# Optimization experiments

Hardware: AMD Instinct MI355X
Metric: run time of the kernel (lower is better)

Reference implementation:

```python
import jax, jax.numpy as jnp
import numpy as np

B, C, H, W = 2, 128, 64, 64
HEADS, DHEAD = 4, 32
K = 7           # kernel_size (dilation = 1)
GROUPS = 32
EPS = 1e-5
DA = HEADS * DHEAD


def setup_inputs() -> dict:
    key = jax.random.key(0)
    ks = jax.random.split(key, 8)
    s = lambda k, sh: jax.random.normal(k, sh, jnp.float32) * 0.02
    return {
        "x": jax.random.normal(ks[0], (B, C, H, W), jnp.float32),
        "gn_weight": jnp.ones((C,), jnp.float32),
        "gn_bias": jnp.zeros((C,), jnp.float32),
        "wq": s(ks[1], (DA, C)), "bq": jnp.zeros((DA,), jnp.float32),
        "wk": s(ks[2], (DA, C)), "bk": jnp.zeros((DA,), jnp.float32),
        "wv": s(ks[3], (DA, C)), "bv": jnp.zeros((DA,), jnp.float32),
        "wo": s(ks[4], (C, DA)), "bo": jnp.zeros((C,), jnp.float32),
        "rpb": s(ks[5], (HEADS, 2 * K - 1, 2 * K - 1)),
    }


def _win_starts(L):
    # NATTEN window start: clamp so the k-window stays in-bounds
    return jnp.clip(jnp.arange(L) - K // 2, 0, L - K)


def _pb_starts(L):
    # NATTEN relative-position-bias start index along one axis
    idx = jnp.arange(L)
    ns = K // 2
    return ns + jnp.maximum(ns - idx, 0) + jnp.minimum(L - idx - 1 - ns, 0)


def reference(x, gn_weight, gn_bias, wq, bq, wk, bk, wv, bv, wo, bo, rpb):
    Bn, Cn, Hn, Wn = x.shape
    # GroupNorm (biased variance, like torch)
    xg = x.reshape(Bn, GROUPS, -1)
    mu = xg.mean(-1, keepdims=True)
    var = xg.var(-1, keepdims=True)
    xg = (xg - mu) * jax.lax.rsqrt(var + EPS)
    xn = xg.reshape(Bn, Cn, Hn, Wn) * gn_weight[:, None, None] + gn_bias[:, None, None]

    def proj(w, b):
        # 1x1 conv == channel matmul; -> (B, heads, H, W, d)
        y = jnp.einsum('bchw,oc->bohw', xn, w) + b[:, None, None]
        return y.reshape(Bn, HEADS, DHEAD, Hn, Wn).transpose(0, 1, 3, 4, 2)

    q = proj(wq, bq) * (DHEAD ** -0.5)
    k = proj(wk, bk)
    v = proj(wv, bv)

    off = jnp.arange(K)
    ih = _win_starts(Hn)[:, None] + off        # (H, K) neighbor rows
    iw = _win_starts(Wn)[:, None] + off        # (W, K) neighbor cols
    # gathered windows: (B, heads, H, W, K, K, d)
    kw = k[:, :, ih[:, None, :, None], iw[None, :, None, :], :]
    vw = v[:, :, ih[:, None, :, None], iw[None, :, None, :], :]

    bh = _pb_starts(Hn)[:, None] + off         # (H, K)
    bw = _pb_starts(Wn)[:, None] + off         # (W, K)
    bias = rpb[:, bh[:, None, :, None], bw[None, :, None, :]]  # (heads, H, W, K, K)

    attn = jnp.einsum('nhpqd,nhpqijd->nhpqij', q, kw) + bias[None]
    attn = jax.nn.softmax(attn.reshape(Bn, HEADS, Hn, Wn, K * K), axis=-1)
    attn = attn.reshape(Bn, HEADS, Hn, Wn, K, K)
    out = jnp.einsum('nhpqij,nhpqijd->nhpqd', attn, vw)  # (B, heads, H, W, d)
    # faithful to the torch code: raw reshape (B,heads,H,W,d)->(B,H,W,heads*d)
    xo = out.reshape(Bn, Hn, Wn, HEADS * DHEAD).transpose(0, 3, 1, 2)
    return jnp.einsum('bchw,oc->bohw', xo, wo) + bo[:, None, None]
```

## Files before the change

### kernel.cpp

```cpp
#include <hip/hip_runtime.h>

#define EPS 1e-5f

typedef short s8v __attribute__((ext_vector_type(8)));
typedef float f4v __attribute__((ext_vector_type(4)));

static __device__ inline short f2bf(float f) {
  return __builtin_bit_cast(short, (__bf16)f);
}

#define OFF_S     0
#define OFF_T     256
#define OFF_WCB   512
#define OFF_BC    (OFF_WCB + 24576)
#define OFF_QB    (OFF_BC + 384)
#define OFF_KB    (OFF_QB + 524288)
#define OFF_VTB   (OFF_KB + 524288)
#define OFF_WOB   (OFF_VTB + 524288)

__global__ __launch_bounds__(256) void kP(
    const float* __restrict__ wq, const float* __restrict__ bq,
    const float* __restrict__ wk, const float* __restrict__ bk,
    const float* __restrict__ wv, const float* __restrict__ bv,
    const float* __restrict__ wo, const float* __restrict__ gw,
    const float* __restrict__ gb, const float* __restrict__ x,
    short* __restrict__ Wcb, float* __restrict__ bc,
    short* __restrict__ WoB, float* __restrict__ sArr, float* __restrict__ tArr) {
  int blk = blockIdx.x;
  if (blk < 64) {
    int t = blk * 256 + threadIdx.x;
    const float qs = 0.17677669529663687f;
    Wcb[t]         = f2bf(wq[t] * qs);
    Wcb[16384 + t] = f2bf(wk[t]);
    Wcb[32768 + t] = f2bf(wv[t]);
    WoB[t]         = f2bf(wo[t]);
    if (t < 128) {
      bc[t]       = bq[t] * qs;
      bc[128 + t] = bk[t];
      bc[256 + t] = bv[t];
    }
  } else {
    int g = blk - 64;
    const float4* xp = (const float4*)(x + (size_t)g * 16384);
    float s = 0.f, s2 = 0.f;
    for (int i = threadIdx.x; i < 4096; i += 256) {
      float4 v = xp[i];
      s  += v.x + v.y + v.z + v.w;
      s2 += v.x*v.x + v.y*v.y + v.z*v.z + v.w*v.w;
    }
    #pragma unroll
    for (int o = 32; o; o >>= 1) {
      s  += __shfl_down(s, o, 64);
      s2 += __shfl_down(s2, o, 64);
    }
    __shared__ float ls[4], ls2[4];
    int wid = threadIdx.x >> 6, lane = threadIdx.x & 63;
    if (!lane) { ls[wid] = s; ls2[wid] = s2; }
    __syncthreads();
    if (threadIdx.x == 0) {
      float S = 0.f, S2 = 0.f;
      #pragma unroll
      for (int i = 0; i < 4; i++) { S += ls[i]; S2 += ls2[i]; }
      float mean = S * (1.f / 16384.f);
      float var  = S2 * (1.f / 16384.f) - mean * mean;
      float rsv  = rsqrtf(var + EPS);
      int b = g >> 5, grp = g & 31;
      #pragma unroll
      for (int j = 0; j < 4; j++) {
        int c = grp * 4 + j;
        float sv = rsv * gw[c];
        sArr[b * 128 + c] = sv;
        tArr[b * 128 + c] = gb[c] - mean * sv;
      }
    }
  }
}

__global__ __launch_bounds__(256) void k2_qkv(
    const float* __restrict__ x, const float* __restrict__ sArr, const float* __restrict__ tArr,
    const short* __restrict__ Wcb, const float* __restrict__ bc,
    short* __restrict__ qb, short* __restrict__ kb, short* __restrict__ vtb) {
  __shared__ short xn[64][136];
  __shared__ short WL[192][136];
  __shared__ float bcs[192];
  int bid    = blockIdx.x;
  int ptile  = bid >> 1, nslice = bid & 1;
  int b      = ptile >> 6;
  int pbase  = (ptile & 63) * 64;
  int nbase  = nslice * 192;
  int tid    = threadIdx.x;
  int w      = __builtin_amdgcn_readfirstlane(tid >> 6);
  int lane   = tid & 63;

  #pragma unroll
  for (int i = 0; i < 16; i++) {
    int c0 = (w + i * 4) * 2;
    float s0 = sArr[b * 128 + c0],     t0 = tArr[b * 128 + c0];
    float s1 = sArr[b * 128 + c0 + 1], t1 = tArr[b * 128 + c0 + 1];
    float v0 = x[((size_t)(b * 128 + c0))     * 4096 + pbase + lane];
    float v1 = x[((size_t)(b * 128 + c0 + 1)) * 4096 + pbase + lane];
    ushort e0 = (ushort)f2bf(fmaf(v0, s0, t0));
    ushort e1 = (ushort)f2bf(fmaf(v1, s1, t1));
    *(uint*)&xn[lane][c0] = ((uint)e1 << 16) | e0;
  }
  #pragma unroll
  for (int i = 0; i < 12; i++) {
    int cc = tid + i * 256;
    int row = cc >> 4, c8 = (cc & 15) * 8;
    *(s8v*)&WL[row][c8] = *(const s8v*)&Wcb[(nbase + row) * 128 + c8];
  }
  if (tid < 192) bcs[tid] = bc[nbase + tid];
  __syncthreads();

  int l15 = lane & 15, kh = lane >> 4;
  f4v acc[12];
  #pragma unroll
  for (int nt = 0; nt < 12; nt++) acc[nt] = (f4v){0.f, 0.f, 0.f, 0.f};
  #pragma unroll
  for (int ks = 0; ks < 4; ks++) {
    s8v a = *(s8v*)&xn[w * 16 + l15][ks * 32 + kh * 8];
    #pragma unroll
    for (int nt = 0; nt < 12; nt++) {
      s8v wf = *(s8v*)&WL[nt * 16 + l15][ks * 32 + kh * 8];
      if (nbase + nt * 16 < 256)
        acc[nt] = __builtin_amdgcn_mfma_f32_16x16x32_bf16(wf, a, acc[nt], 0, 0, 0);
      else
        acc[nt] = __builtin_amdgcn_mfma_f32_16x16x32_bf16(a, wf, acc[nt], 0, 0, 0);
    }
  }
  #pragma unroll
  for (int nt = 0; nt < 12; nt++) {
    if (nbase + nt * 16 < 256) {
      int ob  = nt * 16 + kh * 4;
      int o0i = nbase + ob;
      int hd  = (o0i & 127) >> 5, d0 = o0i & 31;
      int bh2 = b * 4 + hd;
      int px  = pbase + w * 16 + l15;
      short* dst = (o0i >> 7) ? kb : qb;
      ushort e0 = (ushort)f2bf(acc[nt][0] + bcs[ob + 0]);
      ushort e1 = (ushort)f2bf(acc[nt][1] + bcs[ob + 1]);
      ushort e2 = (ushort)f2bf(acc[nt][2] + bcs[ob + 2]);
      ushort e3 = (ushort)f2bf(acc[nt][3] + bcs[ob + 3]);
      uint2 pk = make_uint2(((uint)e1 << 16) | e0, ((uint)e3 << 16) | e2);
      *(uint2*)&dst[((size_t)bh2 * 4096 + px) * 32 + d0] = pk;
    } else {
      int o   = nbase + nt * 16 + l15;
      int hd  = (o & 127) >> 5, d = o & 31;
      int bh2 = b * 4 + hd;
      int px0 = pbase + w * 16 + kh * 4;
      float bias = bcs[nt * 16 + l15];
      ushort s0 = (ushort)f2bf(acc[nt][0] + bias);
      ushort s1 = (ushort)f2bf(acc[nt][1] + bias);
      ushort s2 = (ushort)f2bf(acc[nt][2] + bias);
      ushort s3 = (ushort)f2bf(acc[nt][3] + bias);
      uint2 pk2 = make_uint2(((uint)s1 << 16) | s0, ((uint)s3 << 16) | s2);
      *(uint2*)&vtb[((size_t)bh2 * 32 + d) * 4096 + px0] = pk2;
    }
  }
}

__global__ __launch_bounds__(512) void k3_attn_proj(
    const short* __restrict__ qb, const short* __restrict__ kb, const short* __restrict__ vtb,
    const float* __restrict__ rpb, const short* __restrict__ WoB,
    const float* __restrict__ bo, float* __restrict__ out) {
  struct PhA { ushort K[8][64][32]; ushort VT[8][32][68]; ushort P[8][16][40]; float rpb[176]; };
  struct PhB { ushort tile[2][16][136]; ushort Wo[128][136]; };
  __shared__ union { PhA a; PhB bb; } sm;

  int lb    = blockIdx.x;
  int bh    = lb & 7;
  int chunk = lb >> 3;
  int y0    = chunk * 2;
  int head  = bh & 3, b = bh >> 2;
  int tid   = threadIdx.x;
  int w     = __builtin_amdgcn_readfirstlane(tid >> 6);
  int lane  = tid & 63, l15 = lane & 15, kh = lane >> 4;
  int wsub  = w & 3, rsel = w >> 2;
  int y     = y0 + rsel;
  int ys0   = min(max(y0 - 3, 0), 57);
  int ysoff = min(max(y - 3, 0), 57) - ys0;

  {
    const size_t kbase = (size_t)bh * 4096 * 32;
    #pragma unroll
    for (int i = 0; i < 4; i++) {
      int cc = tid + i * 512;
      int row = cc >> 8, rem = cc & 255;
      int col = rem >> 2, ch8 = (rem & 3) * 8;
      int yr = min(ys0 + row, 63);
      *(s8v*)&sm.a.K[row][col][ch8] = *(const s8v*)&kb[kbase + (size_t)(yr * 64 + col) * 32 + ch8];
    }
  }
  {
    const size_t vbase = (size_t)bh * 32 * 4096;
    #pragma unroll
    for (int i = 0; i < 4; i++) {
      int cc = tid + i * 512;
      int row = cc >> 8, rem = cc & 255;
      int d = rem >> 3, c8 = (rem & 7) * 8;
      int yr = min(ys0 + row, 63);
      *(s8v*)&sm.a.VT[row][d][c8] = *(const s8v*)&vtb[vbase + (size_t)d * 4096 + yr * 64 + c8];
    }
  }
  if (tid < 169) sm.a.rpb[tid] = rpb[head * 169 + tid];
  __syncthreads();

  int c0  = wsub * 8 + (wsub >> 1) * 8;
  int xq  = wsub * 16 + l15;
  int xs  = min(max(xq - 3, 0), 57);
  int pbw = 3 + max(3 - xq, 0) + min(60 - xq, 0);
  int pbh = 3 + max(3 - y, 0) + min(60 - y, 0);

  s8v qf = *(const s8v*)&qb[((size_t)bh * 4096 + y * 64 + xq) * 32 + kh * 8];

  int   bidx[8];
  float badd[8];
  #pragma unroll
  for (int j = 0; j < 8; ++j) {
    int cc = (j >> 2) * 16 + kh * 4 + (j & 3);
    int dx = c0 + cc - xs;
    bool valid = (dx >= 0) && (dx < 7);
    bidx[j] = pbw + min(max(dx, 0), 6);
    badd[j] = valid ? 0.f : -1e30f;
  }

  const f4v zero = {0.f, 0.f, 0.f, 0.f};
  f4v o0 = zero, o1 = zero;
  float ssum = 0.f;

  #pragma unroll
  for (int row = 0; row < 7; ++row) {
    int kr = ysoff + row;
    s8v ka0 = *(s8v*)&sm.a.K[kr][c0 + l15][kh * 8];
    s8v ka1 = *(s8v*)&sm.a.K[kr][c0 + 16 + l15][kh * 8];
    f4v lg0 = __builtin_amdgcn_mfma_f32_16x16x32_bf16(ka0, qf, zero, 0, 0, 0);
    f4v lg1 = __builtin_amdgcn_mfma_f32_16x16x32_bf16(ka1, qf, zero, 0, 0, 0);
    int rbase = (pbh + row) * 13;
    float p[8];
    #pragma unroll
    for (int j = 0; j < 4; ++j) {
      p[j]     = __expf(lg0[j] + sm.a.rpb[rbase + bidx[j]]     + badd[j]);
      p[j + 4] = __expf(lg1[j] + sm.a.rpb[rbase + bidx[j + 4]] + badd[j + 4]);
      ssum += p[j] + p[j + 4];
    }
    uint u0 = ((uint)(ushort)f2bf(p[1]) << 16) | (ushort)f2bf(p[0]);
    uint u1 = ((uint)(ushort)f2bf(p[3]) << 16) | (ushort)f2bf(p[2]);
    uint u2 = ((uint)(ushort)f2bf(p[5]) << 16) | (ushort)f2bf(p[4]);
    uint u3 = ((uint)(ushort)f2bf(p[7]) << 16) | (ushort)f2bf(p[6]);
    *(uint2*)&sm.a.P[w][l15][kh * 4]      = make_uint2(u0, u1);
    *(uint2*)&sm.a.P[w][l15][16 + kh * 4] = make_uint2(u2, u3);
    s8v pa  = *(s8v*)&sm.a.P[w][l15][kh * 8];
    s8v vt0 = *(s8v*)&sm.a.VT[kr][l15][c0 + kh * 8];
    s8v vt1 = *(s8v*)&sm.a.VT[kr][16 + l15][c0 + kh * 8];
    o0 = __builtin_amdgcn_mfma_f32_16x16x32_bf16(pa, vt0, o0, 0, 0, 0);
    o1 = __builtin_amdgcn_mfma_f32_16x16x32_bf16(pa, vt1, o1, 0, 0, 0);
  }

  ssum += __shfl_xor(ssum, 16, 64);
  ssum += __shfl_xor(ssum, 32, 64);

  __syncthreads();

  #pragma unroll
  for (int i = 0; i < 4; i++) {
    int cc = tid + i * 512;
    int row = cc >> 4, c8 = (cc & 15) * 8;
    *(s8v*)&sm.bb.Wo[row][c8] = *(const s8v*)&WoB[row * 128 + c8];
  }
  {
    int col = wsub * 4 + kh;
    #pragma unroll
    for (int r = 0; r < 4; ++r) {
      float sq = __builtin_bit_cast(float,
          __builtin_amdgcn_ds_bpermute((kh * 4 + r) << 2, __builtin_bit_cast(int, ssum)));
      float inv = 1.f / sq;
      sm.bb.tile[rsel][col][r * 32 + l15]      = (ushort)f2bf(o0[r] * inv);
      sm.bb.tile[rsel][col][r * 32 + 16 + l15] = (ushort)f2bf(o1[r] * inv);
    }
  }
  __syncthreads();

  f4v acc2[2];
  acc2[0] = zero; acc2[1] = zero;
  #pragma unroll
  for (int ks = 0; ks < 4; ks++) {
    s8v a = *(s8v*)&sm.bb.tile[rsel][l15][ks * 32 + kh * 8];
    #pragma unroll
    for (int nt = 0; nt < 2; nt++) {
      s8v bf = *(s8v*)&sm.bb.Wo[wsub * 32 + nt * 16 + l15][ks * 32 + kh * 8];
      acc2[nt] = __builtin_amdgcn_mfma_f32_16x16x32_bf16(a, bf, acc2[nt], 0, 0, 0);
    }
  }
  int pxg = (head * 16 + (y >> 2)) * 64 + ((y & 3) << 4);
  #pragma unroll
  for (int nt = 0; nt < 2; nt++) {
    int o = wsub * 32 + nt * 16 + l15;
    float bias = bo[o];
    float4 val = make_float4(acc2[nt][0] + bias, acc2[nt][1] + bias,
                             acc2[nt][2] + bias, acc2[nt][3] + bias);
    *(float4*)&out[((size_t)b * 128 + o) * 4096 + pxg + kh * 4] = val;
  }
}

extern "C" void kernel_launch(void* const* d_in, const int* in_sizes, int n_in,
                              void* d_out, int out_size, void* d_ws, size_t ws_size,
                              hipStream_t stream) {
  (void)in_sizes; (void)n_in; (void)out_size; (void)ws_size;
  const float* x   = (const float*)d_in[0];
  const float* gw  = (const float*)d_in[1];
  const float* gb  = (const float*)d_in[2];
  const float* wq  = (const float*)d_in[3];
  const float* bq  = (const float*)d_in[4];
  const float* wk  = (const float*)d_in[5];
  const float* bk  = (const float*)d_in[6];
  const float* wv  = (const float*)d_in[7];
  const float* bv  = (const float*)d_in[8];
  const float* wo  = (const float*)d_in[9];
  const float* bo  = (const float*)d_in[10];
  const float* rpb = (const float*)d_in[11];
  float* ws    = (float*)d_ws;
  float* sArr  = ws + OFF_S;
  float* tArr  = ws + OFF_T;
  short* Wcb   = (short*)(ws + OFF_WCB);
  float* bc    = ws + OFF_BC;
  short* qb    = (short*)(ws + OFF_QB);
  short* kb    = (short*)(ws + OFF_KB);
  short* vtb   = (short*)(ws + OFF_VTB);
  short* WoB   = (short*)(ws + OFF_WOB);
  float* out   = (float*)d_out;

  hipLaunchKernelGGL(kP, dim3(128), dim3(256), 0, stream,
                     wq, bq, wk, bk, wv, bv, wo, gw, gb, x, Wcb, bc, WoB, sArr, tArr);
  hipLaunchKernelGGL(k2_qkv, dim3(256), dim3(256), 0, stream,
                     x, sArr, tArr, Wcb, bc, qb, kb, vtb);
  hipLaunchKernelGGL(k3_attn_proj, dim3(256), dim3(512), 0, stream,
                     qb, kb, vtb, rpb, WoB, bo, out);
}
```

Baseline: 32.36 us.

## Split GroupNorm stats into partial sums, finalize in QKV kernel, preload Wo

```diff
diff --git a/kernel.cpp b/kernel.cpp
--- a/kernel.cpp
+++ b/kernel.cpp
@@ -9,8 +9,8 @@
   return __builtin_bit_cast(short, (__bf16)f);
 }
 
-#define OFF_S     0
-#define OFF_T     256
+#define OFF_SP    0
+#define OFF_S2P   256
 #define OFF_WCB   512
 #define OFF_BC    (OFF_WCB + 24576)
 #define OFF_QB    (OFF_BC + 384)
@@ -22,13 +22,13 @@
     const float* __restrict__ wq, const float* __restrict__ bq,
     const float* __restrict__ wk, const float* __restrict__ bk,
     const float* __restrict__ wv, const float* __restrict__ bv,
-    const float* __restrict__ wo, const float* __restrict__ gw,
-    const float* __restrict__ gb, const float* __restrict__ x,
+    const float* __restrict__ wo, const float* __restrict__ x,
     short* __restrict__ Wcb, float* __restrict__ bc,
-    short* __restrict__ WoB, float* __restrict__ sArr, float* __restrict__ tArr) {
+    short* __restrict__ WoB, float* __restrict__ Spart, float* __restrict__ S2part) {
   int blk = blockIdx.x;
+  int tid = threadIdx.x;
   if (blk < 64) {
-    int t = blk * 256 + threadIdx.x;
+    int t = blk * 256 + tid;
     const float qs = 0.17677669529663687f;
     Wcb[t]         = f2bf(wq[t] * qs);
     Wcb[16384 + t] = f2bf(wk[t]);
@@ -40,11 +40,13 @@
       bc[256 + t] = bv[t];
     }
   } else {
-    int g = blk - 64;
-    const float4* xp = (const float4*)(x + (size_t)g * 16384);
+    int idx = blk - 64;
+    int g = idx >> 2, part = idx & 3;
+    const float4* xp = (const float4*)(x + (size_t)g * 16384 + part * 4096);
     float s = 0.f, s2 = 0.f;
-    for (int i = threadIdx.x; i < 4096; i += 256) {
-      float4 v = xp[i];
+    #pragma unroll
+    for (int i = 0; i < 4; i++) {
+      float4 v = xp[tid + i * 256];
       s  += v.x + v.y + v.z + v.w;
       s2 += v.x*v.x + v.y*v.y + v.z*v.z + v.w*v.w;
     }
@@ -54,35 +56,29 @@
       s2 += __shfl_down(s2, o, 64);
     }
     __shared__ float ls[4], ls2[4];
-    int wid = threadIdx.x >> 6, lane = threadIdx.x & 63;
+    int wid = tid >> 6, lane = tid & 63;
     if (!lane) { ls[wid] = s; ls2[wid] = s2; }
     __syncthreads();
-    if (threadIdx.x == 0) {
+    if (tid == 0) {
       float S = 0.f, S2 = 0.f;
       #pragma unroll
       for (int i = 0; i < 4; i++) { S += ls[i]; S2 += ls2[i]; }
-      float mean = S * (1.f / 16384.f);
-      float var  = S2 * (1.f / 16384.f) - mean * mean;
-      float rsv  = rsqrtf(var + EPS);
-      int b = g >> 5, grp = g & 31;
-      #pragma unroll
-      for (int j = 0; j < 4; j++) {
-        int c = grp * 4 + j;
-        float sv = rsv * gw[c];
-        sArr[b * 128 + c] = sv;
-        tArr[b * 128 + c] = gb[c] - mean * sv;
-      }
+      Spart[idx]  = S;
+      S2part[idx] = S2;
     }
   }
 }
 
 __global__ __launch_bounds__(256) void k2_qkv(
-    const float* __restrict__ x, const float* __restrict__ sArr, const float* __restrict__ tArr,
+    const float* __restrict__ x,
+    const float* __restrict__ Spart, const float* __restrict__ S2part,
+    const float* __restrict__ gw, const float* __restrict__ gb,
     const short* __restrict__ Wcb, const float* __restrict__ bc,
     short* __restrict__ qb, short* __restrict__ kb, short* __restrict__ vtb) {
   __shared__ short xn[64][136];
   __shared__ short WL[192][136];
   __shared__ float bcs[192];
+  __shared__ float sm_s[128], sm_t[128];
   int bid    = blockIdx.x;
   int ptile  = bid >> 1, nslice = bid & 1;
   int b      = ptile >> 6;
@@ -92,16 +88,22 @@
   int w      = __builtin_amdgcn_readfirstlane(tid >> 6);
   int lane   = tid & 63;
 
+  float va[16], vb[16];
   #pragma unroll
   for (int i = 0; i < 16; i++) {
     int c0 = (w + i * 4) * 2;
-    float s0 = sArr[b * 128 + c0],     t0 = tArr[b * 128 + c0];
-    float s1 = sArr[b * 128 + c0 + 1], t1 = tArr[b * 128 + c0 + 1];
-    float v0 = x[((size_t)(b * 128 + c0))     * 4096 + pbase + lane];
-    float v1 = x[((size_t)(b * 128 + c0 + 1)) * 4096 + pbase + lane];
-    ushort e0 = (ushort)f2bf(fmaf(v0, s0, t0));
-    ushort e1 = (ushort)f2bf(fmaf(v1, s1, t1));
-    *(uint*)&xn[lane][c0] = ((uint)e1 << 16) | e0;
+    va[i] = x[((size_t)(b * 128 + c0))     * 4096 + pbase + lane];
+    vb[i] = x[((size_t)(b * 128 + c0 + 1)) * 4096 + pbase + lane];
+  }
+  if (tid < 128) {
+    int c = tid, gi = (b * 32 + (c >> 2)) * 4;
+    float S  = Spart[gi]  + Spart[gi + 1]  + Spart[gi + 2]  + Spart[gi + 3];
+    float S2 = S2part[gi] + S2part[gi + 1] + S2part[gi + 2] + S2part[gi + 3];
+    float mean = S * (1.f / 16384.f);
+    float var  = S2 * (1.f / 16384.f) - mean * mean;
+    float sv   = rsqrtf(var + EPS) * gw[c];
+    sm_s[c] = sv;
+    sm_t[c] = gb[c] - mean * sv;
   }
   #pragma unroll
   for (int i = 0; i < 12; i++) {
@@ -110,6 +112,15 @@
     *(s8v*)&WL[row][c8] = *(const s8v*)&Wcb[(nbase + row) * 128 + c8];
   }
   if (tid < 192) bcs[tid] = bc[nbase + tid];
+  __syncthreads();
+
+  #pragma unroll
+  for (int i = 0; i < 16; i++) {
+    int c0 = (w + i * 4) * 2;
+    ushort e0 = (ushort)f2bf(fmaf(va[i], sm_s[c0],     sm_t[c0]));
+    ushort e1 = (ushort)f2bf(fmaf(vb[i], sm_s[c0 + 1], sm_t[c0 + 1]));
+    *(uint*)&xn[lane][c0] = ((uint)e1 << 16) | e0;
+  }
   __syncthreads();
 
   int l15 = lane & 15, kh = lane >> 4;
@@ -163,9 +174,12 @@
     const short* __restrict__ qb, const short* __restrict__ kb, const short* __restrict__ vtb,
     const float* __restrict__ rpb, const short* __restrict__ WoB,
     const float* __restrict__ bo, float* __restrict__ out) {
-  struct PhA { ushort K[8][64][32]; ushort VT[8][32][68]; ushort P[8][16][40]; float rpb[176]; };
-  struct PhB { ushort tile[2][16][136]; ushort Wo[128][136]; };
-  __shared__ union { PhA a; PhB bb; } sm;
+  __shared__ ushort K_s[8][64][32];
+  __shared__ ushort VT_s[8][32][68];
+  __shared__ ushort P_s[8][16][40];
+  __shared__ ushort Wo_s[128][136];
+  __shared__ ushort tile_s[2][16][136];
+  __shared__ float  rpb_s[176];
 
   int lb    = blockIdx.x;
   int bh    = lb & 7;
@@ -188,7 +202,7 @@
       int row = cc >> 8, rem = cc & 255;
       int col = rem >> 2, ch8 = (rem & 3) * 8;
       int yr = min(ys0 + row, 63);
-      *(s8v*)&sm.a.K[row][col][ch8] = *(const s8v*)&kb[kbase + (size_t)(yr * 64 + col) * 32 + ch8];
+      *(s8v*)&K_s[row][col][ch8] = *(const s8v*)&kb[kbase + (size_t)(yr * 64 + col) * 32 + ch8];
     }
   }
   {
@@ -199,10 +213,16 @@
       int row = cc >> 8, rem = cc & 255;
       int d = rem >> 3, c8 = (rem & 7) * 8;
       int yr = min(ys0 + row, 63);
-      *(s8v*)&sm.a.VT[row][d][c8] = *(const s8v*)&vtb[vbase + (size_t)d * 4096 + yr * 64 + c8];
-    }
-  }
-  if (tid < 169) sm.a.rpb[tid] = rpb[head * 169 + tid];
+      *(s8v*)&VT_s[row][d][c8] = *(const s8v*)&vtb[vbase + (size_t)d * 4096 + yr * 64 + c8];
+    }
+  }
+  #pragma unroll
+  for (int i = 0; i < 4; i++) {
+    int cc = tid + i * 512;
+    int row = cc >> 4, c8 = (cc & 15) * 8;
+    *(s8v*)&Wo_s[row][c8] = *(const s8v*)&WoB[row * 128 + c8];
+  }
+  if (tid < 169) rpb_s[tid] = rpb[head * 169 + tid];
   __syncthreads();
 
   int c0  = wsub * 8 + (wsub >> 1) * 8;
@@ -231,27 +251,27 @@
   #pragma unroll
   for (int row = 0; row < 7; ++row) {
     int kr = ysoff + row;
-    s8v ka0 = *(s8v*)&sm.a.K[kr][c0 + l15][kh * 8];
-    s8v ka1 = *(s8v*)&sm.a.K[kr][c0 + 16 + l15][kh * 8];
+    s8v ka0 = *(s8v*)&K_s[kr][c0 + l15][kh * 8];
+    s8v ka1 = *(s8v*)&K_s[kr][c0 + 16 + l15][kh * 8];
     f4v lg0 = __builtin_amdgcn_mfma_f32_16x16x32_bf16(ka0, qf, zero, 0, 0, 0);
     f4v lg1 = __builtin_amdgcn_mfma_f32_16x16x32_bf16(ka1, qf, zero, 0, 0, 0);
     int rbase = (pbh + row) * 13;
     float p[8];
     #pragma unroll
     for (int j = 0; j < 4; ++j) {
-      p[j]     = __expf(lg0[j] + sm.a.rpb[rbase + bidx[j]]     + badd[j]);
-      p[j + 4] = __expf(lg1[j] + sm.a.rpb[rbase + bidx[j + 4]] + badd[j + 4]);
+      p[j]     = __expf(lg0[j] + rpb_s[rbase + bidx[j]]     + badd[j]);
+      p[j + 4] = __expf(lg1[j] + rpb_s[rbase + bidx[j + 4]] + badd[j + 4]);
       ssum += p[j] + p[j + 4];
     }
     uint u0 = ((uint)(ushort)f2bf(p[1]) << 16) | (ushort)f2bf(p[0]);
     uint u1 = ((uint)(ushort)f2bf(p[3]) << 16) | (ushort)f2bf(p[2]);
     uint u2 = ((uint)(ushort)f2bf(p[5]) << 16) | (ushort)f2bf(p[4]);
     uint u3 = ((uint)(ushort)f2bf(p[7]) << 16) | (ushort)f2bf(p[6]);
-    *(uint2*)&sm.a.P[w][l15][kh * 4]      = make_uint2(u0, u1);
-    *(uint2*)&sm.a.P[w][l15][16 + kh * 4] = make_uint2(u2, u3);
-    s8v pa  = *(s8v*)&sm.a.P[w][l15][kh * 8];
-    s8v vt0 = *(s8v*)&sm.a.VT[kr][l15][c0 + kh * 8];
-    s8v vt1 = *(s8v*)&sm.a.VT[kr][16 + l15][c0 + kh * 8];
+    *(uint2*)&P_s[w][l15][kh * 4]      = make_uint2(u0, u1);
+    *(uint2*)&P_s[w][l15][16 + kh * 4] = make_uint2(u2, u3);
+    s8v pa  = *(s8v*)&P_s[w][l15][kh * 8];
+    s8v vt0 = *(s8v*)&VT_s[kr][l15][c0 + kh * 8];
+    s8v vt1 = *(s8v*)&VT_s[kr][16 + l15][c0 + kh * 8];
     o0 = __builtin_amdgcn_mfma_f32_16x16x32_bf16(pa, vt0, o0, 0, 0, 0);
     o1 = __builtin_amdgcn_mfma_f32_16x16x32_bf16(pa, vt1, o1, 0, 0, 0);
   }
@@ -259,14 +279,6 @@
   ssum += __shfl_xor(ssum, 16, 64);
   ssum += __shfl_xor(ssum, 32, 64);
 
-  __syncthreads();
-
-  #pragma unroll
-  for (int i = 0; i < 4; i++) {
-    int cc = tid + i * 512;
-    int row = cc >> 4, c8 = (cc & 15) * 8;
-    *(s8v*)&sm.bb.Wo[row][c8] = *(const s8v*)&WoB[row * 128 + c8];
-  }
   {
     int col = wsub * 4 + kh;
     #pragma unroll
@@ -274,8 +286,8 @@
       float sq = __builtin_bit_cast(float,
           __builtin_amdgcn_ds_bpermute((kh * 4 + r) << 2, __builtin_bit_cast(int, ssum)));
       float inv = 1.f / sq;
-      sm.bb.tile[rsel][col][r * 32 + l15]      = (ushort)f2bf(o0[r] * inv);
-      sm.bb.tile[rsel][col][r * 32 + 16 + l15] = (ushort)f2bf(o1[r] * inv);
+      tile_s[rsel][col][r * 32 + l15]      = (ushort)f2bf(o0[r] * inv);
+      tile_s[rsel][col][r * 32 + 16 + l15] = (ushort)f2bf(o1[r] * inv);
     }
   }
   __syncthreads();
@@ -284,10 +296,10 @@
   acc2[0] = zero; acc2[1] = zero;
   #pragma unroll
   for (int ks = 0; ks < 4; ks++) {
-    s8v a = *(s8v*)&sm.bb.tile[rsel][l15][ks * 32 + kh * 8];
+    s8v a = *(s8v*)&tile_s[rsel][l15][ks * 32 + kh * 8];
     #pragma unroll
     for (int nt = 0; nt < 2; nt++) {
-      s8v bf = *(s8v*)&sm.bb.Wo[wsub * 32 + nt * 16 + l15][ks * 32 + kh * 8];
+      s8v bf = *(s8v*)&Wo_s[wsub * 32 + nt * 16 + l15][ks * 32 + kh * 8];
       acc2[nt] = __builtin_amdgcn_mfma_f32_16x16x32_bf16(a, bf, acc2[nt], 0, 0, 0);
     }
   }
@@ -318,21 +330,21 @@
   const float* wo  = (const float*)d_in[9];
   const float* bo  = (const float*)d_in[10];
   const float* rpb = (const float*)d_in[11];
-  float* ws    = (float*)d_ws;
-  float* sArr  = ws + OFF_S;
-  float* tArr  = ws + OFF_T;
-  short* Wcb   = (short*)(ws + OFF_WCB);
-  float* bc    = ws + OFF_BC;
-  short* qb    = (short*)(ws + OFF_QB);
-  short* kb    = (short*)(ws + OFF_KB);
-  short* vtb   = (short*)(ws + OFF_VTB);
-  short* WoB   = (short*)(ws + OFF_WOB);
-  float* out   = (float*)d_out;
-
-  hipLaunchKernelGGL(kP, dim3(128), dim3(256), 0, stream,
-                     wq, bq, wk, bk, wv, bv, wo, gw, gb, x, Wcb, bc, WoB, sArr, tArr);
+  float* ws     = (float*)d_ws;
+  float* Spart  = ws + OFF_SP;
+  float* S2part = ws + OFF_S2P;
+  short* Wcb    = (short*)(ws + OFF_WCB);
+  float* bc     = ws + OFF_BC;
+  short* qb     = (short*)(ws + OFF_QB);
+  short* kb     = (short*)(ws + OFF_KB);
+  short* vtb    = (short*)(ws + OFF_VTB);
+  short* WoB    = (short*)(ws + OFF_WOB);
+  float* out    = (float*)d_out;
+
+  hipLaunchKernelGGL(kP, dim3(320), dim3(256), 0, stream,
+                     wq, bq, wk, bk, wv, bv, wo, x, Wcb, bc, WoB, Spart, S2part);
   hipLaunchKernelGGL(k2_qkv, dim3(256), dim3(256), 0, stream,
-                     x, sArr, tArr, Wcb, bc, qb, kb, vtb);
+                     x, Spart, S2part, gw, gb, Wcb, bc, qb, kb, vtb);
   hipLaunchKernelGGL(k3_attn_proj, dim3(256), dim3(512), 0, stream,
                      qb, kb, vtb, rpb, WoB, bo, out);
 }
```

Measured after the change: 26.96 us. 1.2x faster.
